# Kernel optimization log

Measured on AMD Instinct MI355X. Metric: run time of the kernel, lower is better.

The kernel has to match this reference:

```python
import jax, jax.numpy as jnp
import numpy as np

NS, NT, DF, H, O = 200000, 50000, 20, 64, 64
NE, NL = 1000000, 500000


def setup_inputs() -> dict:
    key = jax.random.key(0)
    ks = jax.random.split(key, 24)
    inp = {
        'target_x': jax.random.normal(ks[0], (NT, DF), jnp.float32),
        'source_node_id': jnp.arange(NS, dtype=jnp.int64),
        'target_node_id': jnp.arange(NT, dtype=jnp.int64),
        'edge_src': jax.random.randint(ks[1], (NE,), 0, NS),
        'edge_dst': jax.random.randint(ks[2], (NE,), 0, NT),
        'label_src': jax.random.randint(ks[3], (NL,), 0, NS),
        'label_dst': jax.random.randint(ks[4], (NL,), 0, NT),
        'src_emb': jax.random.normal(ks[5], (NS, H), jnp.float32) * 0.05,
        'tgt_emb': jax.random.normal(ks[6], (NT, H), jnp.float32) * 0.05,
        'lin_W': jax.random.normal(ks[7], (DF, H), jnp.float32) * 0.05,
        'lin_b': jnp.zeros((H,), jnp.float32),
    }
    # SAGEConv params: (Wl, bl, Wr) per edge type per layer. st = source->target, ts = target->source
    dims = {'st1': (H, H), 'ts1': (H, H), 'st2': (H, O), 'ts2': (H, O)}
    i = 8
    for name, (din, dout) in dims.items():
        inp['Wl_' + name] = jax.random.normal(ks[i], (din, dout), jnp.float32) * 0.05
        inp['bl_' + name] = jnp.zeros((dout,), jnp.float32)
        inp['Wr_' + name] = jax.random.normal(ks[i + 1], (din, dout), jnp.float32) * 0.05
        i += 2
    return inp


def _sage(x_src, x_dst, src_idx, dst_idx, n_dst, Wl, bl, Wr):
    # PyG SAGEConv, aggr='mean': lin_l(mean_{j in N(i)} x_j) + lin_r(x_i)
    msg = x_src[src_idx]                                   # [E, d] gather
    agg = jax.ops.segment_sum(msg, dst_idx, num_segments=n_dst)
    deg = jax.ops.segment_sum(jnp.ones((src_idx.shape[0],), x_src.dtype), dst_idx, num_segments=n_dst)
    mean = agg / jnp.maximum(deg, 1.0)[:, None]
    return mean @ Wl + bl + x_dst @ Wr


def reference(target_x, source_node_id, target_node_id, edge_src, edge_dst,
              label_src, label_dst, src_emb, tgt_emb, lin_W, lin_b,
              Wl_st1, bl_st1, Wr_st1, Wl_ts1, bl_ts1, Wr_ts1,
              Wl_st2, bl_st2, Wr_st2, Wl_ts2, bl_ts2, Wr_ts2):
    ns, nt = src_emb.shape[0], tgt_emb.shape[0]
    x_s = src_emb[source_node_id]                          # [NS, H]
    x_t = target_x @ lin_W + lin_b + tgt_emb[target_node_id]  # [NT, H]
    # layer 1 (per edge type, summed per dst type; each dst type has one incoming type)
    h_t = _sage(x_s, x_t, edge_src, edge_dst, nt, Wl_st1, bl_st1, Wr_st1)
    h_s = _sage(x_t, x_s, edge_dst, edge_src, ns, Wl_ts1, bl_ts1, Wr_ts1)
    h_t, h_s = jax.nn.relu(h_t), jax.nn.relu(h_s)
    # layer 2
    o_t = _sage(h_s, h_t, edge_src, edge_dst, nt, Wl_st2, bl_st2, Wr_st2)
    o_s = _sage(h_t, h_s, edge_dst, edge_src, ns, Wl_ts2, bl_ts2, Wr_ts2)
    # dot-product link classifier
    return (o_s[label_src] * o_t[label_dst]).sum(axis=-1)  # [NL]
```

## Files before the change

kernel.cpp:

```cpp
#include <hip/hip_runtime.h>

#define NSRC 200000
#define NTGT 50000
#define DF   20
#define HD   64
#define NE   1000000
#define NL   500000

#define SH_T 6
#define SH_S 8
#define NB_T ((NTGT + 63) >> 6)
#define NB_S ((NSRC + 255) >> 8)
#define CHUNK 8192

typedef unsigned short ushort_t;
typedef short s16x8 __attribute__((ext_vector_type(8)));
typedef float f32x4 __attribute__((ext_vector_type(4)));

__device__ __forceinline__ float bf2f(ushort_t u) {
    return __uint_as_float(((unsigned)u) << 16);
}
__device__ __forceinline__ ushort_t f2bf(float f) {
    unsigned u = __float_as_uint(f);
    return (ushort_t)((u + 0x7fffu + ((u >> 16) & 1u)) >> 16);
}

__global__ __launch_bounds__(256) void bin_count(
    const int* __restrict__ es, const int* __restrict__ ed,
    int* __restrict__ bcnt_t, int* __restrict__ bcnt_s, int ne)
{
    __shared__ int ht[NB_T];
    __shared__ int hs[NB_S];
    for (int i = threadIdx.x; i < NB_T; i += 256) ht[i] = 0;
    for (int i = threadIdx.x; i < NB_S; i += 256) hs[i] = 0;
    __syncthreads();
    const int stride = gridDim.x * 256;
    for (int e = blockIdx.x * 256 + threadIdx.x; e < ne; e += stride) {
        atomicAdd(&ht[ed[e] >> SH_T], 1);
        atomicAdd(&hs[es[e] >> SH_S], 1);
    }
    __syncthreads();
    for (int i = threadIdx.x; i < NB_T; i += 256) { int v = ht[i]; if (v) atomicAdd(&bcnt_t[i], v); }
    for (int i = threadIdx.x; i < NB_S; i += 256) { int v = hs[i]; if (v) atomicAdd(&bcnt_s[i], v); }
}

__global__ __launch_bounds__(1024) void bucket_scan(
    const int* __restrict__ bcnt_t, int* __restrict__ bb_t, int* __restrict__ cur_t,
    const int* __restrict__ bcnt_s, int* __restrict__ bb_s, int* __restrict__ cur_s,
    int nb)
{
    const int* bcnt = blockIdx.x ? bcnt_s : bcnt_t;
    int* bb  = blockIdx.x ? bb_s  : bb_t;
    int* cur = blockIdx.x ? cur_s : cur_t;

    __shared__ int s[1024];
    const int tid = threadIdx.x;
    int v = (tid < nb) ? bcnt[tid] : 0;
    s[tid] = v;
    __syncthreads();
    for (int d = 1; d < 1024; d <<= 1) {
        int t = (tid >= d) ? s[tid - d] : 0;
        __syncthreads();
        s[tid] += t;
        __syncthreads();
    }
    int incl = s[tid];
    if (tid < nb) { int ex = incl - v; bb[tid] = ex; cur[tid] = ex; }
    if (tid == nb - 1) bb[nb] = incl;
}

__global__ __launch_bounds__(256) void bin_fill(
    const int* __restrict__ es, const int* __restrict__ ed, int ne,
    int* __restrict__ cur_t, int* __restrict__ cur_s,
    int2* __restrict__ pairs_t, int2* __restrict__ pairs_s)
{
    __shared__ int lt[NB_T];
    __shared__ int ls[NB_S];
    const int base = blockIdx.x * CHUNK;
    const int n = min(CHUNK, ne - base);

    for (int i = threadIdx.x; i < NB_T; i += 256) lt[i] = 0;
    for (int i = threadIdx.x; i < NB_S; i += 256) ls[i] = 0;
    __syncthreads();

    for (int i = threadIdx.x; i < n; i += 256) {
        atomicAdd(&lt[ed[base + i] >> SH_T], 1);
        atomicAdd(&ls[es[base + i] >> SH_S], 1);
    }
    __syncthreads();

    for (int i = threadIdx.x; i < NB_T; i += 256) {
        int c = lt[i];
        lt[i] = c ? atomicAdd(&cur_t[i], c) : 0;
    }
    for (int i = threadIdx.x; i < NB_S; i += 256) {
        int c = ls[i];
        ls[i] = c ? atomicAdd(&cur_s[i], c) : 0;
    }
    __syncthreads();

    for (int i = threadIdx.x; i < n; i += 256) {
        int s = es[base + i], d = ed[base + i];
        int pt = atomicAdd(&lt[d >> SH_T], 1);
        pairs_t[pt] = make_int2(s, d);
        int ps = atomicAdd(&ls[s >> SH_S], 1);
        pairs_s[ps] = make_int2(d, s);
    }
}

template <int SHIFT>
__global__ __launch_bounds__(256) void bucket_build(
    const int2* __restrict__ pairs, const int* __restrict__ bb,
    int* __restrict__ rp, int* __restrict__ col, int n, int ne)
{
    __shared__ int hist[256];
    __shared__ int scn[256];
    __shared__ int cur[256];
    const int b = blockIdx.x;
    const int tid = threadIdx.x;
    const int beg = bb[b], end = bb[b + 1];
    const int row0 = b << SHIFT;

    hist[tid] = 0;
    __syncthreads();
    for (int e = beg + tid; e < end; e += 256)
        atomicAdd(&hist[pairs[e].y - row0], 1);
    __syncthreads();

    int v = hist[tid];
    scn[tid] = v;
    __syncthreads();
    for (int d = 1; d < 256; d <<= 1) {
        int t = (tid >= d) ? scn[tid - d] : 0;
        __syncthreads();
        scn[tid] += t;
        __syncthreads();
    }
    int ex = scn[tid] - v;
    cur[tid] = ex;
    int row = row0 + tid;
    if (tid < (1 << SHIFT) && row < n) rp[row] = beg + ex;
    if (b == 0 && tid == 0) rp[n] = ne;
    __syncthreads();

    for (int e = beg + tid; e < end; e += 256) {
        int2 pr = pairs[e];
        int p = atomicAdd(&cur[pr.y - row0], 1);
        col[beg + p] = pr.x;
    }
}

__global__ void compute_xt(const float* __restrict__ tx, const float* __restrict__ W,
                           const float* __restrict__ b, const float* __restrict__ temb,
                           ushort_t* __restrict__ xb)
{
    int stride = gridDim.x * blockDim.x;
    for (int i = blockIdx.x * blockDim.x + threadIdx.x; i < NTGT * HD; i += stride) {
        int n = i >> 6, k = i & 63;
        float acc = b[k] + temb[i];
#pragma unroll
        for (int d = 0; d < DF; ++d) acc += tx[n * DF + d] * W[d * HD + k];
        xb[i] = f2bf(acc);
    }
}

__global__ void to_bf16(const float* __restrict__ in, ushort_t* __restrict__ out, int n)
{
    int stride = gridDim.x * blockDim.x;
    for (int i = blockIdx.x * blockDim.x + threadIdx.x; i < n; i += stride)
        out[i] = f2bf(in[i]);
}

__global__ void pack_weights(
    const float* __restrict__ Wl0, const float* __restrict__ Wr0,
    const float* __restrict__ Wl1, const float* __restrict__ Wr1,
    const float* __restrict__ Wl2, const float* __restrict__ Wr2,
    const float* __restrict__ Wl3, const float* __restrict__ Wr3,
    ushort_t* __restrict__ wt)
{
    int i = blockIdx.x * blockDim.x + threadIdx.x;
    if (i >= 4 * 64 * 128) return;
    int set = i >> 13, rem = i & 8191;
    int j = rem >> 7, k = rem & 127;
    const float* Wl = set == 0 ? Wl0 : set == 1 ? Wl1 : set == 2 ? Wl2 : Wl3;
    const float* Wr = set == 0 ? Wr0 : set == 1 ? Wr1 : set == 2 ? Wr2 : Wr3;
    float v = (k < 64) ? Wl[k * 64 + j] : Wr[(k - 64) * 64 + j];
    wt[i] = f2bf(v);
}

__global__ __launch_bounds__(256) void aggregate_q(
    const ushort_t* __restrict__ table, const int* __restrict__ rp,
    const int* __restrict__ col, ushort_t* __restrict__ mean, int n_dst)
{
    const int ql = threadIdx.x & 15;
    const int qw = threadIdx.x >> 4;
    const int d0 = ql * 4;
    const int stride = gridDim.x * 16;

#define ACC(S, V)                                                   \
    S.x += bf2f(V.x); S.y += bf2f(V.y); S.z += bf2f(V.z); S.w += bf2f(V.w);

    for (int node = blockIdx.x * 16 + qw; node < n_dst; node += stride) {
        const int beg = rp[node], end = rp[node + 1];
        float4 s0 = make_float4(0.f, 0.f, 0.f, 0.f);
        float4 s1 = make_float4(0.f, 0.f, 0.f, 0.f);
        float4 s2 = make_float4(0.f, 0.f, 0.f, 0.f);
        float4 s3 = make_float4(0.f, 0.f, 0.f, 0.f);
        int e = beg;
        for (; e + 4 <= end; e += 4) {
            int c0 = col[e], c1 = col[e + 1], c2 = col[e + 2], c3 = col[e + 3];
            ushort4 v0 = *(const ushort4*)&table[(size_t)c0 * HD + d0];
            ushort4 v1 = *(const ushort4*)&table[(size_t)c1 * HD + d0];
            ushort4 v2 = *(const ushort4*)&table[(size_t)c2 * HD + d0];
            ushort4 v3 = *(const ushort4*)&table[(size_t)c3 * HD + d0];
            ACC(s0, v0) ACC(s1, v1) ACC(s2, v2) ACC(s3, v3)
        }
        for (; e < end; ++e) {
            ushort4 v = *(const ushort4*)&table[(size_t)col[e] * HD + d0];
            ACC(s0, v)
        }
#undef ACC
        float degf = (float)(end - beg);
        float inv  = degf > 0.f ? 1.f / degf : 0.f;
        ushort4 o;
        o.x = f2bf((s0.x + s1.x + s2.x + s3.x) * inv);
        o.y = f2bf((s0.y + s1.y + s2.y + s3.y) * inv);
        o.z = f2bf((s0.z + s1.z + s2.z + s3.z) * inv);
        o.w = f2bf((s0.w + s1.w + s2.w + s3.w) * inv);
        *(ushort4*)&mean[(size_t)node * HD + d0] = o;
    }
}

template <bool RELU>
__global__ __launch_bounds__(256) void transform_m(
    const ushort_t* __restrict__ mean, const ushort_t* __restrict__ xd,
    const ushort_t* __restrict__ wt,
    const float* __restrict__ bl, ushort_t* __restrict__ out, int n)
{
    const int lane = threadIdx.x & 63;
    const int wid  = threadIdx.x >> 6;
    const int lr   = lane & 15;
    const int kg   = lane >> 4;

    s16x8 b[4][4];
#pragma unroll
    for (int jb = 0; jb < 4; ++jb)
#pragma unroll
        for (int kb = 0; kb < 4; ++kb)
            b[jb][kb] = *(const s16x8*)&wt[(jb * 16 + lr) * 128 + kb * 32 + kg * 8];

    float bias[4];
#pragma unroll
    for (int jb = 0; jb < 4; ++jb) bias[jb] = bl[jb * 16 + lr];

    const int ntiles = (n + 63) >> 6;
    for (int tile = blockIdx.x; tile < ntiles; tile += gridDim.x) {
        const int arow = tile * 64 + wid * 16 + lr;
        s16x8 a[4];
        if (arow < n) {
            const ushort_t* mrow = mean + (size_t)arow * HD;
            const ushort_t* xrow = xd   + (size_t)arow * HD;
            a[0] = *(const s16x8*)(mrow + kg * 8);
            a[1] = *(const s16x8*)(mrow + 32 + kg * 8);
            a[2] = *(const s16x8*)(xrow + kg * 8);
            a[3] = *(const s16x8*)(xrow + 32 + kg * 8);
        } else {
            s16x8 z = {0, 0, 0, 0, 0, 0, 0, 0};
            a[0] = z; a[1] = z; a[2] = z; a[3] = z;
        }

        const int drow0 = tile * 64 + wid * 16 + kg * 4;
#pragma unroll
        for (int jb = 0; jb < 4; ++jb) {
            f32x4 acc = {bias[jb], bias[jb], bias[jb], bias[jb]};
#pragma unroll
            for (int kb = 0; kb < 4; ++kb)
                acc = __builtin_amdgcn_mfma_f32_16x16x32_bf16(a[kb], b[jb][kb], acc, 0, 0, 0);
#pragma unroll
            for (int r = 0; r < 4; ++r) {
                int nn = drow0 + r;
                if (nn < n) {
                    float v = acc[r];
                    if (RELU) v = fmaxf(v, 0.f);
                    out[(size_t)nn * HD + jb * 16 + lr] = f2bf(v);
                }
            }
        }
    }
}

__global__ __launch_bounds__(256) void classify_b(
    const ushort_t* __restrict__ os, const ushort_t* __restrict__ ot,
    const int* __restrict__ ls, const int* __restrict__ lt,
    float* __restrict__ out, int nl)
{
    const int lane = threadIdx.x & 63;
    const int sub  = lane >> 4;
    const int g    = (lane & 15) * 4;
    int w = (blockIdx.x * blockDim.x + threadIdx.x) >> 6;
    const int wstride = (gridDim.x * blockDim.x) >> 6;

    for (int l0 = w * 8; l0 < nl; l0 += wstride * 8) {
        int la = l0 + sub;
        int lb = l0 + 4 + sub;
        float pa = 0.f, pb = 0.f;
        if (la < nl) {
            int a = ls[la], b = lt[la];
            ushort4 va = *(const ushort4*)&os[(size_t)a * HD + g];
            ushort4 vb = *(const ushort4*)&ot[(size_t)b * HD + g];
            pa = bf2f(va.x) * bf2f(vb.x) + bf2f(va.y) * bf2f(vb.y)
               + bf2f(va.z) * bf2f(vb.z) + bf2f(va.w) * bf2f(vb.w);
        }
        if (lb < nl) {
            int a = ls[lb], b = lt[lb];
            ushort4 va = *(const ushort4*)&os[(size_t)a * HD + g];
            ushort4 vb = *(const ushort4*)&ot[(size_t)b * HD + g];
            pb = bf2f(va.x) * bf2f(vb.x) + bf2f(va.y) * bf2f(vb.y)
               + bf2f(va.z) * bf2f(vb.z) + bf2f(va.w) * bf2f(vb.w);
        }
#pragma unroll
        for (int o = 8; o > 0; o >>= 1) {
            pa += __shfl_xor(pa, o, 64);
            pb += __shfl_xor(pb, o, 64);
        }
        if ((lane & 15) == 0) {
            if (la < nl) out[la] = pa;
            if (lb < nl) out[lb] = pb;
        }
    }
}

extern "C" void kernel_launch(void* const* d_in, const int* in_sizes, int n_in,
                              void* d_out, int out_size, void* d_ws, size_t ws_size,
                              hipStream_t stream)
{
    const float* target_x = (const float*)d_in[0];
    const int* edge_src  = (const int*)d_in[3];
    const int* edge_dst  = (const int*)d_in[4];
    const int* label_src = (const int*)d_in[5];
    const int* label_dst = (const int*)d_in[6];
    const float* src_emb = (const float*)d_in[7];
    const float* tgt_emb = (const float*)d_in[8];
    const float* lin_W   = (const float*)d_in[9];
    const float* lin_b   = (const float*)d_in[10];
    const float* Wl_st1 = (const float*)d_in[11];
    const float* bl_st1 = (const float*)d_in[12];
    const float* Wr_st1 = (const float*)d_in[13];
    const float* Wl_ts1 = (const float*)d_in[14];
    const float* bl_ts1 = (const float*)d_in[15];
    const float* Wr_ts1 = (const float*)d_in[16];
    const float* Wl_st2 = (const float*)d_in[17];
    const float* bl_st2 = (const float*)d_in[18];
    const float* Wr_st2 = (const float*)d_in[19];
    const float* Wl_ts2 = (const float*)d_in[20];
    const float* bl_ts2 = (const float*)d_in[21];
    const float* Wr_ts2 = (const float*)d_in[22];
    float* out = (float*)d_out;

    char* ws = (char*)d_ws;
    size_t off = 0;
    auto take = [&](size_t bytes) -> char* {
        char* p = ws + off;
        off = (off + bytes + 255) & ~(size_t)255;
        return p;
    };
    int* bcnt   = (int*)take((size_t)(NB_T + NB_S) * 4);
    int* bcnt_t = bcnt;
    int* bcnt_s = bcnt + NB_T;
    int* bb_t  = (int*)take((size_t)(NB_T + 1) * 4);
    int* bb_s  = (int*)take((size_t)(NB_S + 1) * 4);
    int* cur_t = (int*)take((size_t)NB_T * 4);
    int* cur_s = (int*)take((size_t)NB_S * 4);
    int* rp_t  = (int*)take((size_t)(NTGT + 1) * 4);
    int* rp_s  = (int*)take((size_t)(NSRC + 1) * 4);
    int* col_t = (int*)take((size_t)NE * 4);
    int* col_s = (int*)take((size_t)NE * 4);
    ushort_t* wt   = (ushort_t*)take((size_t)4 * 64 * 128 * 2);
    ushort_t* xb_t = (ushort_t*)take((size_t)NTGT * HD * 2);
    ushort_t* sb   = (ushort_t*)take((size_t)NSRC * HD * 2);
    ushort_t* hb_t = (ushort_t*)take((size_t)NTGT * HD * 2);
    ushort_t* hb_s = (ushort_t*)take((size_t)NSRC * HD * 2);
    ushort_t* mb_t = (ushort_t*)take((size_t)NTGT * HD * 2);
    ushort_t* mb_s = (ushort_t*)take((size_t)NSRC * HD * 2);
    ushort_t* ob_t = mb_t;
    ushort_t* ob_s = mb_s;
    int2* pairs_t = (int2*)mb_s;
    int2* pairs_s = pairs_t + NE;

    hipMemsetAsync(bcnt, 0, (size_t)(NB_T + NB_S) * 4, stream);
    bin_count<<<256, 256, 0, stream>>>(edge_src, edge_dst, bcnt_t, bcnt_s, NE);
    bucket_scan<<<2, 1024, 0, stream>>>(bcnt_t, bb_t, cur_t, bcnt_s, bb_s, cur_s, NB_T);
    bin_fill<<<(NE + CHUNK - 1) / CHUNK, 256, 0, stream>>>(edge_src, edge_dst, NE,
                                                           cur_t, cur_s, pairs_t, pairs_s);
    bucket_build<SH_T><<<NB_T, 256, 0, stream>>>(pairs_t, bb_t, rp_t, col_t, NTGT, NE);
    bucket_build<SH_S><<<NB_S, 256, 0, stream>>>(pairs_s, bb_s, rp_s, col_s, NSRC, NE);

    pack_weights<<<128, 256, 0, stream>>>(Wl_st1, Wr_st1, Wl_ts1, Wr_ts1,
                                          Wl_st2, Wr_st2, Wl_ts2, Wr_ts2, wt);
    compute_xt<<<2048, 256, 0, stream>>>(target_x, lin_W, lin_b, tgt_emb, xb_t);
    to_bf16<<<2048, 256, 0, stream>>>(src_emb, sb, NSRC * HD);

    aggregate_q<<<2048, 256, 0, stream>>>(sb,   rp_t, col_t, mb_t, NTGT);
    aggregate_q<<<2048, 256, 0, stream>>>(xb_t, rp_s, col_s, mb_s, NSRC);
    transform_m<true><<<782, 256, 0, stream>>>(mb_t, xb_t, wt + 0 * 8192, bl_st1, hb_t, NTGT);
    transform_m<true><<<3125, 256, 0, stream>>>(mb_s, sb, wt + 1 * 8192, bl_ts1, hb_s, NSRC);

    aggregate_q<<<2048, 256, 0, stream>>>(hb_s, rp_t, col_t, mb_t, NTGT);
    aggregate_q<<<2048, 256, 0, stream>>>(hb_t, rp_s, col_s, mb_s, NSRC);
    transform_m<false><<<782, 256, 0, stream>>>(mb_t, hb_t, wt + 2 * 8192, bl_st2, ob_t, NTGT);
    transform_m<false><<<3125, 256, 0, stream>>>(mb_s, hb_s, wt + 3 * 8192, bl_ts2, ob_s, NSRC);

    classify_b<<<2048, 256, 0, stream>>>(ob_s, ob_t, label_src, label_dst, out, NL);
}
```

Measured before the change: 329.6 us.

## Use per-chunk histograms for deterministic binning and widen aggregation loads to 16 bytes

Edge binning is restructured so that each chunk writes its own bucket histogram, and a per-bucket scan across chunks then gives every chunk a precomputed offset. This replaces the global atomic cursor reservation and removes the memset. Each direction now runs as its own grid row with 1024-thread blocks. Separately, the mean-aggregation kernel gives each node 8 lanes that each load 8 bf16 values (16 bytes), where it previously used 16 lanes with 8-byte loads. This doubles the nodes per block and cuts the number of load instructions, at the cost of more accumulator registers per thread.

```diff
diff --git a/kernel.cpp b/kernel.cpp
--- a/kernel.cpp
+++ b/kernel.cpp
@@ -9,9 +9,9 @@
 
 #define SH_T 6
 #define SH_S 8
-#define NB_T ((NTGT + 63) >> 6)
-#define NB_S ((NSRC + 255) >> 8)
+#define NB   782
 #define CHUNK 8192
+#define NCH  ((NE + CHUNK - 1) / CHUNK)
 
 typedef unsigned short ushort_t;
 typedef short s16x8 __attribute__((ext_vector_type(8)));
@@ -25,37 +25,55 @@
     return (ushort_t)((u + 0x7fffu + ((u >> 16) & 1u)) >> 16);
 }
 
-__global__ __launch_bounds__(256) void bin_count(
-    const int* __restrict__ es, const int* __restrict__ ed,
-    int* __restrict__ bcnt_t, int* __restrict__ bcnt_s, int ne)
-{
-    __shared__ int ht[NB_T];
-    __shared__ int hs[NB_S];
-    for (int i = threadIdx.x; i < NB_T; i += 256) ht[i] = 0;
-    for (int i = threadIdx.x; i < NB_S; i += 256) hs[i] = 0;
-    __syncthreads();
-    const int stride = gridDim.x * 256;
-    for (int e = blockIdx.x * 256 + threadIdx.x; e < ne; e += stride) {
-        atomicAdd(&ht[ed[e] >> SH_T], 1);
-        atomicAdd(&hs[es[e] >> SH_S], 1);
-    }
-    __syncthreads();
-    for (int i = threadIdx.x; i < NB_T; i += 256) { int v = ht[i]; if (v) atomicAdd(&bcnt_t[i], v); }
-    for (int i = threadIdx.x; i < NB_S; i += 256) { int v = hs[i]; if (v) atomicAdd(&bcnt_s[i], v); }
+__global__ __launch_bounds__(1024) void chunk_hist(
+    const int* __restrict__ es, const int* __restrict__ ed, int ne,
+    int* __restrict__ cnt_t, int* __restrict__ cnt_s)
+{
+    __shared__ int h[NB];
+    const int dir  = blockIdx.y;
+    const int c    = blockIdx.x;
+    const int base = c * CHUNK;
+    const int n    = min(CHUNK, ne - base);
+    const int* key = dir ? es : ed;
+    const int sh   = dir ? SH_S : SH_T;
+    int* cnt       = dir ? cnt_s : cnt_t;
+
+    for (int i = threadIdx.x; i < NB; i += 1024) h[i] = 0;
+    __syncthreads();
+    for (int i = threadIdx.x; i < n; i += 1024)
+        atomicAdd(&h[key[base + i] >> sh], 1);
+    __syncthreads();
+    for (int i = threadIdx.x; i < NB; i += 1024) cnt[c * NB + i] = h[i];
+}
+
+__global__ __launch_bounds__(1024) void chunk_scan(
+    int* __restrict__ cnt_t, int* __restrict__ cnt_s,
+    int* __restrict__ bt_t, int* __restrict__ bt_s)
+{
+    int* cnt = blockIdx.x ? cnt_s : cnt_t;
+    int* bt  = blockIdx.x ? bt_s  : bt_t;
+    const int b = threadIdx.x;
+    if (b < NB) {
+        int run = 0;
+        for (int c = 0; c < NCH; ++c) {
+            int v = cnt[c * NB + b];
+            cnt[c * NB + b] = run;
+            run += v;
+        }
+        bt[b] = run;
+    }
 }
 
 __global__ __launch_bounds__(1024) void bucket_scan(
-    const int* __restrict__ bcnt_t, int* __restrict__ bb_t, int* __restrict__ cur_t,
-    const int* __restrict__ bcnt_s, int* __restrict__ bb_s, int* __restrict__ cur_s,
-    int nb)
-{
-    const int* bcnt = blockIdx.x ? bcnt_s : bcnt_t;
-    int* bb  = blockIdx.x ? bb_s  : bb_t;
-    int* cur = blockIdx.x ? cur_s : cur_t;
+    const int* __restrict__ bt_t, int* __restrict__ bb_t,
+    const int* __restrict__ bt_s, int* __restrict__ bb_s)
+{
+    const int* bt = blockIdx.x ? bt_s : bt_t;
+    int* bb       = blockIdx.x ? bb_s : bb_t;
 
     __shared__ int s[1024];
     const int tid = threadIdx.x;
-    int v = (tid < nb) ? bcnt[tid] : 0;
+    int v = (tid < NB) ? bt[tid] : 0;
     s[tid] = v;
     __syncthreads();
     for (int d = 1; d < 1024; d <<= 1) {
@@ -65,46 +83,35 @@
         __syncthreads();
     }
     int incl = s[tid];
-    if (tid < nb) { int ex = incl - v; bb[tid] = ex; cur[tid] = ex; }
-    if (tid == nb - 1) bb[nb] = incl;
-}
-
-__global__ __launch_bounds__(256) void bin_fill(
+    if (tid < NB) bb[tid] = incl - v;
+    if (tid == NB - 1) bb[NB] = incl;
+}
+
+__global__ __launch_bounds__(1024) void bin_fill2(
     const int* __restrict__ es, const int* __restrict__ ed, int ne,
-    int* __restrict__ cur_t, int* __restrict__ cur_s,
+    const int* __restrict__ cnt_t, const int* __restrict__ cnt_s,
+    const int* __restrict__ bb_t, const int* __restrict__ bb_s,
     int2* __restrict__ pairs_t, int2* __restrict__ pairs_s)
 {
-    __shared__ int lt[NB_T];
-    __shared__ int ls[NB_S];
-    const int base = blockIdx.x * CHUNK;
-    const int n = min(CHUNK, ne - base);
-
-    for (int i = threadIdx.x; i < NB_T; i += 256) lt[i] = 0;
-    for (int i = threadIdx.x; i < NB_S; i += 256) ls[i] = 0;
-    __syncthreads();
-
-    for (int i = threadIdx.x; i < n; i += 256) {
-        atomicAdd(&lt[ed[base + i] >> SH_T], 1);
-        atomicAdd(&ls[es[base + i] >> SH_S], 1);
-    }
-    __syncthreads();
-
-    for (int i = threadIdx.x; i < NB_T; i += 256) {
-        int c = lt[i];
-        lt[i] = c ? atomicAdd(&cur_t[i], c) : 0;
-    }
-    for (int i = threadIdx.x; i < NB_S; i += 256) {
-        int c = ls[i];
-        ls[i] = c ? atomicAdd(&cur_s[i], c) : 0;
-    }
-    __syncthreads();
-
-    for (int i = threadIdx.x; i < n; i += 256) {
-        int s = es[base + i], d = ed[base + i];
-        int pt = atomicAdd(&lt[d >> SH_T], 1);
-        pairs_t[pt] = make_int2(s, d);
-        int ps = atomicAdd(&ls[s >> SH_S], 1);
-        pairs_s[ps] = make_int2(d, s);
+    __shared__ int cur[NB];
+    const int dir  = blockIdx.y;
+    const int c    = blockIdx.x;
+    const int base = c * CHUNK;
+    const int n    = min(CHUNK, ne - base);
+    const int* key = dir ? es : ed;
+    const int* oth = dir ? ed : es;
+    const int sh   = dir ? SH_S : SH_T;
+    const int* cnt = dir ? cnt_s : cnt_t;
+    const int* bb  = dir ? bb_s  : bb_t;
+    int2* pairs    = dir ? pairs_s : pairs_t;
+
+    for (int i = threadIdx.x; i < NB; i += 1024)
+        cur[i] = bb[i] + cnt[c * NB + i];
+    __syncthreads();
+    for (int i = threadIdx.x; i < n; i += 1024) {
+        int k = key[base + i], o = oth[base + i];
+        int p = atomicAdd(&cur[k >> sh], 1);
+        pairs[p] = make_int2(o, k);
     }
 }
 
@@ -188,46 +195,47 @@
     wt[i] = f2bf(v);
 }
 
-__global__ __launch_bounds__(256) void aggregate_q(
+__global__ __launch_bounds__(256) void aggregate_o(
     const ushort_t* __restrict__ table, const int* __restrict__ rp,
     const int* __restrict__ col, ushort_t* __restrict__ mean, int n_dst)
 {
-    const int ql = threadIdx.x & 15;
-    const int qw = threadIdx.x >> 4;
-    const int d0 = ql * 4;
-    const int stride = gridDim.x * 16;
-
-#define ACC(S, V)                                                   \
-    S.x += bf2f(V.x); S.y += bf2f(V.y); S.z += bf2f(V.z); S.w += bf2f(V.w);
-
-    for (int node = blockIdx.x * 16 + qw; node < n_dst; node += stride) {
+    const int el = threadIdx.x & 7;
+    const int ew = threadIdx.x >> 3;
+    const int d0 = el * 8;
+    const int stride = gridDim.x * 32;
+
+    for (int node = blockIdx.x * 32 + ew; node < n_dst; node += stride) {
         const int beg = rp[node], end = rp[node + 1];
-        float4 s0 = make_float4(0.f, 0.f, 0.f, 0.f);
-        float4 s1 = make_float4(0.f, 0.f, 0.f, 0.f);
-        float4 s2 = make_float4(0.f, 0.f, 0.f, 0.f);
-        float4 s3 = make_float4(0.f, 0.f, 0.f, 0.f);
+        float a0[8], a1[8], a2[8], a3[8];
+#pragma unroll
+        for (int i = 0; i < 8; ++i) { a0[i] = 0.f; a1[i] = 0.f; a2[i] = 0.f; a3[i] = 0.f; }
         int e = beg;
         for (; e + 4 <= end; e += 4) {
             int c0 = col[e], c1 = col[e + 1], c2 = col[e + 2], c3 = col[e + 3];
-            ushort4 v0 = *(const ushort4*)&table[(size_t)c0 * HD + d0];
-            ushort4 v1 = *(const ushort4*)&table[(size_t)c1 * HD + d0];
-            ushort4 v2 = *(const ushort4*)&table[(size_t)c2 * HD + d0];
-            ushort4 v3 = *(const ushort4*)&table[(size_t)c3 * HD + d0];
-            ACC(s0, v0) ACC(s1, v1) ACC(s2, v2) ACC(s3, v3)
+            s16x8 v0 = *(const s16x8*)&table[(size_t)c0 * HD + d0];
+            s16x8 v1 = *(const s16x8*)&table[(size_t)c1 * HD + d0];
+            s16x8 v2 = *(const s16x8*)&table[(size_t)c2 * HD + d0];
+            s16x8 v3 = *(const s16x8*)&table[(size_t)c3 * HD + d0];
+#pragma unroll
+            for (int i = 0; i < 8; ++i) {
+                a0[i] += bf2f((ushort_t)v0[i]);
+                a1[i] += bf2f((ushort_t)v1[i]);
+                a2[i] += bf2f((ushort_t)v2[i]);
+                a3[i] += bf2f((ushort_t)v3[i]);
+            }
         }
         for (; e < end; ++e) {
-            ushort4 v = *(const ushort4*)&table[(size_t)col[e] * HD + d0];
-            ACC(s0, v)
-        }
-#undef ACC
+            s16x8 v = *(const s16x8*)&table[(size_t)col[e] * HD + d0];
+#pragma unroll
+            for (int i = 0; i < 8; ++i) a0[i] += bf2f((ushort_t)v[i]);
+        }
         float degf = (float)(end - beg);
         float inv  = degf > 0.f ? 1.f / degf : 0.f;
-        ushort4 o;
-        o.x = f2bf((s0.x + s1.x + s2.x + s3.x) * inv);
-        o.y = f2bf((s0.y + s1.y + s2.y + s3.y) * inv);
-        o.z = f2bf((s0.z + s1.z + s2.z + s3.z) * inv);
-        o.w = f2bf((s0.w + s1.w + s2.w + s3.w) * inv);
-        *(ushort4*)&mean[(size_t)node * HD + d0] = o;
+        s16x8 o;
+#pragma unroll
+        for (int i = 0; i < 8; ++i)
+            o[i] = (short)f2bf((a0[i] + a1[i] + a2[i] + a3[i]) * inv);
+        *(s16x8*)&mean[(size_t)node * HD + d0] = o;
     }
 }
 
@@ -364,13 +372,12 @@
         off = (off + bytes + 255) & ~(size_t)255;
         return p;
     };
-    int* bcnt   = (int*)take((size_t)(NB_T + NB_S) * 4);
-    int* bcnt_t = bcnt;
-    int* bcnt_s = bcnt + NB_T;
-    int* bb_t  = (int*)take((size_t)(NB_T + 1) * 4);
-    int* bb_s  = (int*)take((size_t)(NB_S + 1) * 4);
-    int* cur_t = (int*)take((size_t)NB_T * 4);
-    int* cur_s = (int*)take((size_t)NB_S * 4);
+    int* cnt_t = (int*)take((size_t)NCH * NB * 4);
+    int* cnt_s = (int*)take((size_t)NCH * NB * 4);
+    int* bt_t  = (int*)take((size_t)NB * 4);
+    int* bt_s  = (int*)take((size_t)NB * 4);
+    int* bb_t  = (int*)take((size_t)(NB + 1) * 4);
+    int* bb_s  = (int*)take((size_t)(NB + 1) * 4);
     int* rp_t  = (int*)take((size_t)(NTGT + 1) * 4);
     int* rp_s  = (int*)take((size_t)(NSRC + 1) * 4);
     int* col_t = (int*)take((size_t)NE * 4);
@@ -387,26 +394,27 @@
     int2* pairs_t = (int2*)mb_s;
     int2* pairs_s = pairs_t + NE;
 
-    hipMemsetAsync(bcnt, 0, (size_t)(NB_T + NB_S) * 4, stream);
-    bin_count<<<256, 256, 0, stream>>>(edge_src, edge_dst, bcnt_t, bcnt_s, NE);
-    bucket_scan<<<2, 1024, 0, stream>>>(bcnt_t, bb_t, cur_t, bcnt_s, bb_s, cur_s, NB_T);
-    bin_fill<<<(NE + CHUNK - 1) / CHUNK, 256, 0, stream>>>(edge_src, edge_dst, NE,
-                                                           cur_t, cur_s, pairs_t, pairs_s);
-    bucket_build<SH_T><<<NB_T, 256, 0, stream>>>(pairs_t, bb_t, rp_t, col_t, NTGT, NE);
-    bucket_build<SH_S><<<NB_S, 256, 0, stream>>>(pairs_s, bb_s, rp_s, col_s, NSRC, NE);
+    dim3 gch(NCH, 2);
+    chunk_hist<<<gch, 1024, 0, stream>>>(edge_src, edge_dst, NE, cnt_t, cnt_s);
+    chunk_scan<<<2, 1024, 0, stream>>>(cnt_t, cnt_s, bt_t, bt_s);
+    bucket_scan<<<2, 1024, 0, stream>>>(bt_t, bb_t, bt_s, bb_s);
+    bin_fill2<<<gch, 1024, 0, stream>>>(edge_src, edge_dst, NE,
+                                        cnt_t, cnt_s, bb_t, bb_s, pairs_t, pairs_s);
+    bucket_build<SH_T><<<NB, 256, 0, stream>>>(pairs_t, bb_t, rp_t, col_t, NTGT, NE);
+    bucket_build<SH_S><<<NB, 256, 0, stream>>>(pairs_s, bb_s, rp_s, col_s, NSRC, NE);
 
     pack_weights<<<128, 256, 0, stream>>>(Wl_st1, Wr_st1, Wl_ts1, Wr_ts1,
                                           Wl_st2, Wr_st2, Wl_ts2, Wr_ts2, wt);
     compute_xt<<<2048, 256, 0, stream>>>(target_x, lin_W, lin_b, tgt_emb, xb_t);
     to_bf16<<<2048, 256, 0, stream>>>(src_emb, sb, NSRC * HD);
 
-    aggregate_q<<<2048, 256, 0, stream>>>(sb,   rp_t, col_t, mb_t, NTGT);
-    aggregate_q<<<2048, 256, 0, stream>>>(xb_t, rp_s, col_s, mb_s, NSRC);
+    aggregate_o<<<2048, 256, 0, stream>>>(sb,   rp_t, col_t, mb_t, NTGT);
+    aggregate_o<<<2048, 256, 0, stream>>>(xb_t, rp_s, col_s, mb_s, NSRC);
     transform_m<true><<<782, 256, 0, stream>>>(mb_t, xb_t, wt + 0 * 8192, bl_st1, hb_t, NTGT);
     transform_m<true><<<3125, 256, 0, stream>>>(mb_s, sb, wt + 1 * 8192, bl_ts1, hb_s, NSRC);
 
-    aggregate_q<<<2048, 256, 0, stream>>>(hb_s, rp_t, col_t, mb_t, NTGT);
-    aggregate_q<<<2048, 256, 0, stream>>>(hb_t, rp_s, col_s, mb_s, NSRC);
+    aggregate_o<<<2048, 256, 0, stream>>>(hb_s, rp_t, col_t, mb_t, NTGT);
+    aggregate_o<<<2048, 256, 0, stream>>>(hb_t, rp_s, col_s, mb_s, NSRC);
     transform_m<false><<<782, 256, 0, stream>>>(mb_t, hb_t, wt + 2 * 8192, bl_st2, ob_t, NTGT);
     transform_m<false><<<3125, 256, 0, stream>>>(mb_s, hb_s, wt + 3 * 8192, bl_ts2, ob_s, NSRC);
 
```

After: 312.4 us. 5.2% less time.
